# Kernel tuning notes

Hardware: AMD Instinct MI355X
Metric: run time of the kernel (lower is better)

The kernel has to match this reference:

```python
import jax, jax.numpy as jnp
import numpy as np

W_DIM = 512
IN_CH = 512
OUT_CH = 512
K = 3
PAD = K // 2
LR_MUL = 1.0
WEIGHT_GAIN = LR_MUL / np.sqrt(IN_CH * K * K)
MOD_WEIGHT_GAIN = 1.0 / np.sqrt(W_DIM)  # EqualizedLinear lr_mul=1.0
MOD_BIAS_GAIN = 1.0


def setup_inputs() -> dict:
    key = jax.random.key(0)
    k1, k2, k3, k4 = jax.random.split(key, 4)
    x = jax.random.normal(k1, (16, IN_CH, 64, 64), dtype=jnp.float32)
    w = jax.random.normal(k2, (16, W_DIM), dtype=jnp.float32)
    weight = jax.random.normal(k3, (OUT_CH, IN_CH, K, K), dtype=jnp.float32) / LR_MUL
    mod_weight = jax.random.normal(k4, (IN_CH, W_DIM), dtype=jnp.float32)
    mod_bias = jnp.ones((IN_CH,), dtype=jnp.float32)  # bias_init=1.0
    return {"x": x, "w": w, "weight": weight, "mod_weight": mod_weight, "mod_bias": mod_bias}


def _conv_one(xi, wi):
    # xi: [C_in, H, W], wi: [C_out, C_in, K, K]
    out = jax.lax.conv_general_dilated(
        xi[None], wi, window_strides=(1, 1),
        padding=[(PAD, PAD), (PAD, PAD)],
        dimension_numbers=("NCHW", "OIHW", "NCHW"))
    return out[0]


def reference(x, w, weight, mod_weight, mod_bias):
    # style = EqualizedLinear(w): [B, C_in]
    style = w @ (mod_weight * MOD_WEIGHT_GAIN).T + mod_bias * MOD_BIAS_GAIN
    # modulate weights per-sample: [B, C_out, C_in, K, K]
    wmod = (weight * WEIGHT_GAIN)[None] * style[:, None, :, None, None]
    # demodulate
    demod = jax.lax.rsqrt(jnp.sum(jnp.square(wmod), axis=(2, 3, 4), keepdims=True) + 1e-8)
    wmod = wmod * demod
    # per-sample conv (groups=batch in the original) via vmap
    out = jax.vmap(_conv_one)(x, wmod)  # [B, C_out, H, W]
    return out
```

## Files before the change

kernel.cpp:

```cpp
#include <hip/hip_runtime.h>
#include <hip/hip_bf16.h>

#define IN_CH 512
#define OUT_CH 512
#define HW 64
#define BATCH 16
#define WEIGHT_GAIN 0.014731391274719739f
#define MOD_WEIGHT_GAIN 0.04419417382415922f

#define PAD_W 66
#define XS_PIX_STRIDE 512

typedef __attribute__((ext_vector_type(8))) short frag8;
typedef __attribute__((ext_vector_type(4))) float f32x4;

__global__ void style_kernel(const float* __restrict__ w, const float* __restrict__ mw,
                             const float* __restrict__ mb, float* __restrict__ style) {
    const int gw = (blockIdx.x * 256 + threadIdx.x) >> 6;
    const int lane = threadIdx.x & 63;
    const int b = gw >> 9;
    const int i = gw & 511;
    const float4* mwp = (const float4*)(mw + (size_t)i * 512 + lane * 8);
    const float4* wp  = (const float4*)(w + (size_t)b * 512 + lane * 8);
    float4 m0 = mwp[0], m1 = mwp[1];
    float4 w0 = wp[0],  w1 = wp[1];
    float s = m0.x * w0.x + m0.y * w0.y + m0.z * w0.z + m0.w * w0.w
            + m1.x * w1.x + m1.y * w1.y + m1.z * w1.z + m1.w * w1.w;
#pragma unroll
    for (int off = 32; off > 0; off >>= 1) s += __shfl_down(s, off, 64);
    if (lane == 0) style[(size_t)b * 512 + i] = s * MOD_WEIGHT_GAIN + mb[i];
}

__global__ void wprep_kernel(const float* __restrict__ weight, float* __restrict__ wsq,
                             __hip_bfloat16* __restrict__ wbf) {
    const int idx = blockIdx.x * 256 + threadIdx.x;
    const float* wp = weight + idx * 9;
    float s = 0.f;
#pragma unroll
    for (int kk = 0; kk < 9; ++kk) {
        float v = wp[kk];
        s += v * v;
        wbf[kk * 262144 + idx] = __float2bfloat16(v);
    }
    wsq[idx] = s * (WEIGHT_GAIN * WEIGHT_GAIN);
}

__global__ void demod_kernel(const float* __restrict__ style, const float* __restrict__ wsq,
                             float* __restrict__ sc) {
    const int gw = (blockIdx.x * 256 + threadIdx.x) >> 6;
    const int lane = threadIdx.x & 63;
    const int b = gw >> 9;
    const int o = gw & 511;
    const float4* wq = (const float4*)(wsq + (size_t)o * 512 + lane * 8);
    const float4* st = (const float4*)(style + (size_t)b * 512 + lane * 8);
    float4 q0 = wq[0], q1 = wq[1];
    float4 s0 = st[0], s1 = st[1];
    float acc = q0.x * s0.x * s0.x + q0.y * s0.y * s0.y + q0.z * s0.z * s0.z + q0.w * s0.w * s0.w
              + q1.x * s1.x * s1.x + q1.y * s1.y * s1.y + q1.z * s1.z * s1.z + q1.w * s1.w * s1.w;
#pragma unroll
    for (int off = 32; off > 0; off >>= 1) acc += __shfl_down(acc, off, 64);
    if (lane == 0) sc[(size_t)b * 512 + o] = rsqrtf(acc + 1e-8f) * WEIGHT_GAIN;
}

__global__ void xs_kernel(const float* __restrict__ x, const float* __restrict__ style,
                          __hip_bfloat16* __restrict__ xsp) {
    const int b = blockIdx.z;
    const int t = threadIdx.x;
    if (blockIdx.x == 64) {
        const int g = blockIdx.y;
        const int wv = t >> 6, lane = t & 63;
        for (int k = wv; k < 65; k += 4) {
            const int p = g * 65 + k;
            int row, col;
            if (p < 66)       { row = 0;            col = p; }
            else if (p < 132) { row = 65;           col = p - 66; }
            else if (p < 196) { row = p - 132 + 1;  col = 0; }
            else              { row = p - 196 + 1;  col = 65; }
            uint4* dst = (uint4*)(xsp + (((size_t)b * PAD_W + row) * PAD_W + col) * XS_PIX_STRIDE);
            dst[lane] = uint4{0, 0, 0, 0};
        }
        return;
    }
    const int y = blockIdx.x;
    const int lane = t & 63;
    const int j0 = (blockIdx.y * 4 + (t >> 6)) * 32;

    const float* xb = x + (((size_t)b * 512 + j0) * 64 + y) * 64 + lane;
    const float* stb = style + (size_t)b * 512 + j0;
    __hip_bfloat16* dst = xsp + (((size_t)b * PAD_W + (y + 1)) * PAD_W + (lane + 1)) * XS_PIX_STRIDE + j0;

    union { __hip_bfloat16 h[32]; uint4 u[4]; } pk;
#pragma unroll
    for (int k = 0; k < 32; ++k) {
        float v = xb[(size_t)k * 4096];
        pk.h[k] = __float2bfloat16(v * stb[k]);
    }
#pragma unroll
    for (int q = 0; q < 4; ++q) ((uint4*)dst)[q] = pk.u[q];
}

__global__ __launch_bounds__(512, 1) void conv_kernel(const __hip_bfloat16* __restrict__ wbf,
                            const __hip_bfloat16* __restrict__ xsp,
                            const float* __restrict__ sc,
                            float* __restrict__ out) {
    __shared__ char lds[147456];

    const int id = blockIdx.x;
    const int pidx = (id & 7) | (((id >> 4) & 3) << 3);
    const int m0 = ((id >> 3) & 1) << 8;
    const int b  = id >> 6;
    const int p0 = pidx << 7;
    const int y0 = p0 >> 6;
    const int t = threadIdx.x;

    const int r_base = t >> 3;
    const int s_slot = (t & 7) ^ (r_base & 7);
    const size_t abase = (size_t)(m0 + r_base) * 512 + s_slot * 8;
    int pixoff[2];
#pragma unroll
    for (int q = 0; q < 2; ++q) {
        const int rB = q * 64 + r_base;
        const int yy = y0 + (rB >> 6);
        const int xx = rB & 63;
        pixoff[q] = (((b * PAD_W) + yy) * PAD_W + xx) * XS_PIX_STRIDE + s_slot * 8;
    }

    const int wv = t >> 6;
    const int wm = (wv >> 1) * 64;
    const int wn = (wv & 1) * 64;
    const int lane = t & 63;
    const int ln15 = lane & 15;
    const int quad = lane >> 4;

    f32x4 acc[4][4] = {};

#define STAGE(S, R) do {                                                              \
    const int kk_ = (S) >> 3;                                                         \
    const int c0_ = ((S) & 7) << 6;                                                   \
    const __hip_bfloat16* wsrc_ = wbf + kk_ * 262144 + abase + c0_;                   \
    char* Ab_ = lds + (R) * 49152;                                                    \
    _Pragma("unroll")                                                                 \
    for (int q = 0; q < 4; ++q)                                                       \
        __builtin_amdgcn_global_load_lds(                                             \
            (const __attribute__((address_space(1))) unsigned int*)(wsrc_ + q * 32768),\
            (__attribute__((address_space(3))) unsigned int*)(Ab_ + q * 8192 + t * 16),\
            16, 0, 0);                                                                \
    const int shift_ = ((kk_ / 3) * PAD_W + (kk_ % 3)) * XS_PIX_STRIDE;               \
    const __hip_bfloat16* xb_ = xsp + shift_ + c0_;                                   \
    char* Bb_ = lds + (R) * 49152 + 32768;                                            \
    _Pragma("unroll")                                                                 \
    for (int q = 0; q < 2; ++q)                                                       \
        __builtin_amdgcn_global_load_lds(                                             \
            (const __attribute__((address_space(1))) unsigned int*)(xb_ + pixoff[q]), \
            (__attribute__((address_space(3))) unsigned int*)(Bb_ + q * 8192 + t * 16),\
            16, 0, 0);                                                                \
} while (0)

#define COMPUTE(R) do {                                                               \
    const short* Ap_ = (const short*)(lds + (R) * 49152);                             \
    const short* Bp_ = (const short*)(lds + (R) * 49152 + 32768);                     \
    _Pragma("unroll")                                                                 \
    for (int ks = 0; ks < 2; ++ks) {                                                  \
        const int gq = ks * 4 + quad;                                                 \
        frag8 af[4], bfr[4];                                                          \
        _Pragma("unroll")                                                             \
        for (int mt = 0; mt < 4; ++mt) {                                              \
            const int R_ = wm + mt * 16 + ln15;                                       \
            af[mt] = *(const frag8*)(Ap_ + R_ * 64 + ((gq ^ (R_ & 7)) << 3));         \
        }                                                                             \
        _Pragma("unroll")                                                             \
        for (int nt = 0; nt < 4; ++nt) {                                              \
            const int R_ = wn + nt * 16 + ln15;                                       \
            bfr[nt] = *(const frag8*)(Bp_ + R_ * 64 + ((gq ^ (R_ & 7)) << 3));        \
        }                                                                             \
        __builtin_amdgcn_s_setprio(1);                                                \
        _Pragma("unroll")                                                             \
        for (int mt = 0; mt < 4; ++mt)                                                \
            _Pragma("unroll")                                                         \
            for (int nt = 0; nt < 4; ++nt)                                            \
                acc[mt][nt] = __builtin_amdgcn_mfma_f32_16x16x32_bf16(                \
                    af[mt], bfr[nt], acc[mt][nt], 0, 0, 0);                           \
        __builtin_amdgcn_s_setprio(0);                                                \
    }                                                                                 \
} while (0)

#define WAIT6 asm volatile("s_waitcnt vmcnt(6)" ::: "memory")
#define BAR   asm volatile("s_barrier" ::: "memory")

#define ITER_S(RC, RS) do { WAIT6; BAR; STAGE(s + 2, RS); COMPUTE(RC); BAR; ++s; } while (0)
#define ITER_N(RC)     do { WAIT6; BAR;                   COMPUTE(RC); BAR; ++s; } while (0)

    STAGE(0, 0);
    STAGE(1, 1);
    int s = 0;
    while (s < 69) { ITER_S(0, 2); ITER_S(1, 0); ITER_S(2, 1); }
    ITER_S(0, 2);
    ITER_N(1);
    asm volatile("s_waitcnt vmcnt(0)" ::: "memory");
    BAR;
    COMPUTE(2);

#undef ITER_S
#undef ITER_N
#undef WAIT6
#undef BAR
#undef STAGE
#undef COMPUTE

    const float* scb = sc + b * 512;
    float* outb = out + (size_t)b * 512 * 4096;
#pragma unroll
    for (int mt = 0; mt < 4; ++mt) {
        const int mrow = m0 + wm + mt * 16 + quad * 4;
#pragma unroll
        for (int v = 0; v < 4; ++v) {
            const float sv = scb[mrow + v];
            float* orow = outb + (size_t)(mrow + v) * 4096 + p0 + wn + ln15;
#pragma unroll
            for (int nt = 0; nt < 4; ++nt)
                orow[nt * 16] = acc[mt][nt][v] * sv;
        }
    }
}

extern "C" void kernel_launch(void* const* d_in, const int* in_sizes, int n_in,
                              void* d_out, int out_size, void* d_ws, size_t ws_size,
                              hipStream_t stream) {
    (void)in_sizes; (void)n_in; (void)out_size; (void)ws_size;
    const float* x      = (const float*)d_in[0];
    const float* w      = (const float*)d_in[1];
    const float* weight = (const float*)d_in[2];
    const float* mw     = (const float*)d_in[3];
    const float* mb     = (const float*)d_in[4];
    float* out = (float*)d_out;

    char* ws = (char*)d_ws;
    float* style         = (float*)(ws + 0);
    float* sc            = (float*)(ws + 32768);
    float* wsq           = (float*)(ws + 65536);
    __hip_bfloat16* wbf  = (__hip_bfloat16*)(ws + 1114112);
    __hip_bfloat16* xsp  = (__hip_bfloat16*)(ws + 5832704);

    wprep_kernel<<<dim3(1024), dim3(256), 0, stream>>>(weight, wsq, wbf);
    style_kernel<<<dim3(2048), dim3(256), 0, stream>>>(w, mw, mb, style);
    demod_kernel<<<dim3(2048), dim3(256), 0, stream>>>(style, wsq, sc);
    xs_kernel<<<dim3(65, 4, BATCH), dim3(256), 0, stream>>>(x, style, xsp);
    conv_kernel<<<dim3(1024), dim3(512), 0, stream>>>(wbf, xsp, sc, out);
}
```

Measured before the change: 536.1 us.

## Enlarge conv tile to 256x256 with double-buffered split-phase LDS pipeline

The implicit-GEMM conv block tile grows from 256x128 to 256x256. Each wave now owns 128x64 of output, and the grid is halved to 512 blocks, with a remap that assigns blocks to XCDs. The K loop moves from a triple-buffered 48KB stage to a double-buffered 64KB stage. Each k-tile is split into four MFMA phases, with A/B half-tile loads interleaved between them and B fragments held in registers across the phases. This raises operand reuse per LDS byte and global load, at the cost of more accumulator registers, more barriers, and fewer blocks than CUs.

```diff
diff --git a/kernel.cpp b/kernel.cpp
--- a/kernel.cpp
+++ b/kernel.cpp
@@ -103,114 +103,147 @@
                             const __hip_bfloat16* __restrict__ xsp,
                             const float* __restrict__ sc,
                             float* __restrict__ out) {
-    __shared__ char lds[147456];
-
-    const int id = blockIdx.x;
-    const int pidx = (id & 7) | (((id >> 4) & 3) << 3);
-    const int m0 = ((id >> 3) & 1) << 8;
-    const int b  = id >> 6;
-    const int p0 = pidx << 7;
-    const int y0 = p0 >> 6;
+    __shared__ char lds[131072];
+
+    const int bid = blockIdx.x;
+    const int logical = (bid & 7) * 64 + (bid >> 3);
+    const int m0 = (logical & 1) << 8;
+    const int pt = (logical >> 1) & 15;
+    const int b  = logical >> 5;
+    const int p0 = pt << 8;
+    const int y0 = pt << 2;
     const int t = threadIdx.x;
 
     const int r_base = t >> 3;
     const int s_slot = (t & 7) ^ (r_base & 7);
-    const size_t abase = (size_t)(m0 + r_base) * 512 + s_slot * 8;
-    int pixoff[2];
-#pragma unroll
-    for (int q = 0; q < 2; ++q) {
-        const int rB = q * 64 + r_base;
-        const int yy = y0 + (rB >> 6);
-        const int xx = rB & 63;
-        pixoff[q] = (((b * PAD_W) + yy) * PAD_W + xx) * XS_PIX_STRIDE + s_slot * 8;
+    int pixoff[4];
+#pragma unroll
+    for (int i = 0; i < 4; ++i) {
+        const int ri = i * 64 + r_base;
+        const int yy = y0 + (ri >> 6);
+        const int xx = ri & 63;
+        pixoff[i] = (((b * PAD_W) + yy) * PAD_W + xx) * XS_PIX_STRIDE + s_slot * 8;
     }
 
     const int wv = t >> 6;
-    const int wm = (wv >> 1) * 64;
-    const int wn = (wv & 1) * 64;
+    const int wm = (wv >> 2) * 128;
+    const int wn = (wv & 3) * 64;
     const int lane = t & 63;
     const int ln15 = lane & 15;
     const int quad = lane >> 4;
 
-    f32x4 acc[4][4] = {};
-
-#define STAGE(S, R) do {                                                              \
-    const int kk_ = (S) >> 3;                                                         \
-    const int c0_ = ((S) & 7) << 6;                                                   \
-    const __hip_bfloat16* wsrc_ = wbf + kk_ * 262144 + abase + c0_;                   \
-    char* Ab_ = lds + (R) * 49152;                                                    \
+    f32x4 acc[8][4] = {};
+    frag8 bfr[4][2];
+    frag8 af[4];
+    frag8 ag[8];
+
+#define GLL(SRC, DST) __builtin_amdgcn_global_load_lds(                               \
+    (const __attribute__((address_space(1))) unsigned int*)(SRC),                     \
+    (__attribute__((address_space(3))) unsigned int*)(DST), 16, 0, 0)
+
+#define STAGE_A(J, HALF) do {                                                         \
+    const int jA_ = (J);                                                              \
+    const __hip_bfloat16* srcA_ = wbf + (jA_ >> 3) * 262144                           \
+        + (size_t)(m0 + (HALF) * 128 + r_base) * 512 + ((jA_ & 7) << 6) + s_slot * 8; \
+    char* dstA_ = lds + (jA_ & 1) * 65536 + (HALF) * 16384 + t * 16;                  \
+    GLL(srcA_, dstA_);                                                                \
+    GLL(srcA_ + 64 * 512, dstA_ + 8192);                                              \
+} while (0)
+
+#define STAGE_B(J, HALF) do {                                                         \
+    const int jB_ = (J);                                                              \
+    const int kkB_ = jB_ >> 3;                                                        \
+    const __hip_bfloat16* srcB_ = xsp + ((kkB_ / 3) * PAD_W + (kkB_ % 3)) * XS_PIX_STRIDE \
+        + ((jB_ & 7) << 6);                                                           \
+    char* dstB_ = lds + (jB_ & 1) * 65536 + 32768 + (HALF) * 16384 + t * 16;          \
+    GLL(srcB_ + pixoff[(HALF) * 2 + 0], dstB_);                                       \
+    GLL(srcB_ + pixoff[(HALF) * 2 + 1], dstB_ + 8192);                                \
+} while (0)
+
+#define RD_B_ALL(CUR) do {                                                            \
+    const short* Bp_ = (const short*)(lds + (CUR) * 65536 + 32768);                   \
     _Pragma("unroll")                                                                 \
-    for (int q = 0; q < 4; ++q)                                                       \
-        __builtin_amdgcn_global_load_lds(                                             \
-            (const __attribute__((address_space(1))) unsigned int*)(wsrc_ + q * 32768),\
-            (__attribute__((address_space(3))) unsigned int*)(Ab_ + q * 8192 + t * 16),\
-            16, 0, 0);                                                                \
-    const int shift_ = ((kk_ / 3) * PAD_W + (kk_ % 3)) * XS_PIX_STRIDE;               \
-    const __hip_bfloat16* xb_ = xsp + shift_ + c0_;                                   \
-    char* Bb_ = lds + (R) * 49152 + 32768;                                            \
+    for (int nt = 0; nt < 4; ++nt) {                                                  \
+        const int R_ = wn + nt * 16 + ln15;                                           \
+        _Pragma("unroll")                                                             \
+        for (int ks = 0; ks < 2; ++ks)                                                \
+            bfr[nt][ks] = *(const frag8*)(Bp_ + R_ * 64 + (((ks * 4 + quad) ^ (R_ & 7)) << 3)); \
+    }                                                                                 \
+} while (0)
+
+#define RD_A4(CUR, KS, MTH, DST) do {                                                 \
+    const short* Ap_ = (const short*)(lds + (CUR) * 65536);                           \
     _Pragma("unroll")                                                                 \
-    for (int q = 0; q < 2; ++q)                                                       \
-        __builtin_amdgcn_global_load_lds(                                             \
-            (const __attribute__((address_space(1))) unsigned int*)(xb_ + pixoff[q]), \
-            (__attribute__((address_space(3))) unsigned int*)(Bb_ + q * 8192 + t * 16),\
-            16, 0, 0);                                                                \
-} while (0)
-
-#define COMPUTE(R) do {                                                               \
-    const short* Ap_ = (const short*)(lds + (R) * 49152);                             \
-    const short* Bp_ = (const short*)(lds + (R) * 49152 + 32768);                     \
+    for (int mt = 0; mt < 4; ++mt) {                                                  \
+        const int R_ = wm + ((MTH) * 4 + mt) * 16 + ln15;                             \
+        (DST)[mt] = *(const frag8*)(Ap_ + R_ * 64 + ((((KS) * 4 + quad) ^ (R_ & 7)) << 3)); \
+    }                                                                                 \
+} while (0)
+
+#define MFMA_Q(AF, MTH, KS) do {                                                      \
+    __builtin_amdgcn_s_setprio(1);                                                    \
     _Pragma("unroll")                                                                 \
-    for (int ks = 0; ks < 2; ++ks) {                                                  \
-        const int gq = ks * 4 + quad;                                                 \
-        frag8 af[4], bfr[4];                                                          \
+    for (int mt = 0; mt < 4; ++mt)                                                    \
         _Pragma("unroll")                                                             \
-        for (int mt = 0; mt < 4; ++mt) {                                              \
-            const int R_ = wm + mt * 16 + ln15;                                       \
-            af[mt] = *(const frag8*)(Ap_ + R_ * 64 + ((gq ^ (R_ & 7)) << 3));         \
-        }                                                                             \
-        _Pragma("unroll")                                                             \
-        for (int nt = 0; nt < 4; ++nt) {                                              \
-            const int R_ = wn + nt * 16 + ln15;                                       \
-            bfr[nt] = *(const frag8*)(Bp_ + R_ * 64 + ((gq ^ (R_ & 7)) << 3));        \
-        }                                                                             \
-        __builtin_amdgcn_s_setprio(1);                                                \
-        _Pragma("unroll")                                                             \
-        for (int mt = 0; mt < 4; ++mt)                                                \
-            _Pragma("unroll")                                                         \
-            for (int nt = 0; nt < 4; ++nt)                                            \
-                acc[mt][nt] = __builtin_amdgcn_mfma_f32_16x16x32_bf16(                \
-                    af[mt], bfr[nt], acc[mt][nt], 0, 0, 0);                           \
-        __builtin_amdgcn_s_setprio(0);                                                \
-    }                                                                                 \
-} while (0)
-
-#define WAIT6 asm volatile("s_waitcnt vmcnt(6)" ::: "memory")
-#define BAR   asm volatile("s_barrier" ::: "memory")
-
-#define ITER_S(RC, RS) do { WAIT6; BAR; STAGE(s + 2, RS); COMPUTE(RC); BAR; ++s; } while (0)
-#define ITER_N(RC)     do { WAIT6; BAR;                   COMPUTE(RC); BAR; ++s; } while (0)
-
-    STAGE(0, 0);
-    STAGE(1, 1);
-    int s = 0;
-    while (s < 69) { ITER_S(0, 2); ITER_S(1, 0); ITER_S(2, 1); }
-    ITER_S(0, 2);
-    ITER_N(1);
-    asm volatile("s_waitcnt vmcnt(0)" ::: "memory");
-    BAR;
-    COMPUTE(2);
-
-#undef ITER_S
-#undef ITER_N
-#undef WAIT6
+        for (int nt = 0; nt < 4; ++nt)                                                \
+            acc[(MTH) * 4 + mt][nt] = __builtin_amdgcn_mfma_f32_16x16x32_bf16(        \
+                (AF)[mt], bfr[nt][(KS)], acc[(MTH) * 4 + mt][nt], 0, 0, 0);           \
+    __builtin_amdgcn_s_setprio(0);                                                    \
+} while (0)
+
+#define BAR __builtin_amdgcn_s_barrier()
+#define LGKM0 do { asm volatile("s_waitcnt lgkmcnt(0)" ::: "memory");                 \
+                   __builtin_amdgcn_sched_barrier(0); } while (0)
+#define VM6 asm volatile("s_waitcnt vmcnt(6)" ::: "memory")
+#define VM0 asm volatile("s_waitcnt vmcnt(0)" ::: "memory")
+
+#define KTILE(J, CUR, SP1, SP2, VMC) do {                                             \
+                                         \
+    RD_B_ALL(CUR);                                                                    \
+    RD_A4(CUR, 0, 0, af);                                                             \
+    if (SP1) STAGE_A((J) + 1, 1);                                                     \
+    BAR; LGKM0; MFMA_Q(af, 0, 0); BAR;                                                \
+                                                  \
+    RD_A4(CUR, 0, 1, af);                                                             \
+    if (SP2) STAGE_B((J) + 2, 0);                                                     \
+    BAR; LGKM0; MFMA_Q(af, 1, 0); BAR;                                                \
+                                                  \
+    RD_A4(CUR, 1, 0, ag);                                                             \
+    RD_A4(CUR, 1, 1, ag + 4);                                                         \
+    if (SP2) STAGE_B((J) + 2, 1);                                                     \
+    BAR; LGKM0; MFMA_Q(ag, 0, 1); BAR;                                                \
+                                                               \
+    if (SP2) STAGE_A((J) + 2, 0);                                                     \
+    VMC; BAR; MFMA_Q(ag + 4, 1, 1); BAR;                                              \
+} while (0)
+
+    STAGE_B(0, 0); STAGE_B(0, 1); STAGE_A(0, 0); STAGE_A(0, 1);
+    STAGE_B(1, 0); STAGE_B(1, 1); STAGE_A(1, 0);
+    VM6; BAR;
+
+    for (int j = 0; j < 70; j += 2) {
+        KTILE(j, 0, 1, 1, VM6);
+        KTILE(j + 1, 1, 1, 1, VM6);
+    }
+    KTILE(70, 0, 1, 0, VM0);
+    KTILE(71, 1, 0, 0, (void)0);
+
+#undef KTILE
+#undef VM0
+#undef VM6
+#undef LGKM0
 #undef BAR
-#undef STAGE
-#undef COMPUTE
+#undef MFMA_Q
+#undef RD_A4
+#undef RD_B_ALL
+#undef STAGE_B
+#undef STAGE_A
+#undef GLL
 
     const float* scb = sc + b * 512;
     float* outb = out + (size_t)b * 512 * 4096;
 #pragma unroll
-    for (int mt = 0; mt < 4; ++mt) {
+    for (int mt = 0; mt < 8; ++mt) {
         const int mrow = m0 + wm + mt * 16 + quad * 4;
 #pragma unroll
         for (int v = 0; v < 4; ++v) {
@@ -245,5 +278,5 @@
     style_kernel<<<dim3(2048), dim3(256), 0, stream>>>(w, mw, mb, style);
     demod_kernel<<<dim3(2048), dim3(256), 0, stream>>>(style, wsq, sc);
     xs_kernel<<<dim3(65, 4, BATCH), dim3(256), 0, stream>>>(x, style, xsp);
-    conv_kernel<<<dim3(1024), dim3(512), 0, stream>>>(wbf, xsp, sc, out);
-}
+    conv_kernel<<<dim3(512), dim3(512), 0, stream>>>(wbf, xsp, sc, out);
+}
```

After: 490.2 us. -8.6%, faster.
